# Optimization experiments

Measured on AMD Instinct MI355X. Metric: run time of the kernel, lower is better.

The kernel has to match this reference:

```python
import jax, jax.numpy as jnp
import numpy as np

B, L, D, H = 2, 2048, 512, 8
DK = D // H
NEG = -1e18


def setup_inputs() -> dict:
    key = jax.random.key(0)
    ks = jax.random.split(key, 8)
    q = jax.random.normal(ks[0], (B, L, D), dtype=jnp.float32)
    k = jax.random.normal(ks[1], (B, L, D), dtype=jnp.float32)
    v = jax.random.normal(ks[2], (B, L, D), dtype=jnp.float32)
    mask = jax.random.bernoulli(ks[3], 0.1, (B, L, L))  # True = masked
    # qkv_combined: Linear(D, 3D); proj: Linear(D, D). Stored as (in, out).
    W_qkv = jax.random.normal(ks[4], (D, 3 * D), dtype=jnp.float32) / np.sqrt(D)
    b_qkv = jax.random.normal(ks[5], (3 * D,), dtype=jnp.float32) * 0.02
    W_proj = jax.random.normal(ks[6], (D, D), dtype=jnp.float32) / np.sqrt(D)
    b_proj = jax.random.normal(ks[7], (D,), dtype=jnp.float32) * 0.02
    return {"q": q, "k": k, "v": v, "mask": mask,
            "W_qkv": W_qkv, "b_qkv": b_qkv, "W_proj": W_proj, "b_proj": b_proj}


def reference(q, k, v, mask, W_qkv, b_qkv, W_proj, b_proj):
    # NOTE: original module ignores k, v args; Q/K/V all come from q.
    temper = jnp.sqrt(jnp.float32(D))  # sqrt(model_dim), NOT sqrt(d_k)
    qkv = q @ W_qkv + b_qkv                      # [B, L, 3D]
    qq, kk, vv = jnp.split(qkv, 3, axis=-1)      # each [B, L, D]
    # chunk along last dim into H heads then stack at dim 0 -> [H, B, L, DK]
    def split_heads(x):
        return jnp.transpose(x.reshape(B, L, H, DK), (2, 0, 1, 3))
    qh, kh, vh = split_heads(qq), split_heads(kk), split_heads(vv)
    attn = jnp.einsum('hbqd,hbkd->hbqk', qh, kh) / temper  # [H, B, L, L]
    attn = jnp.where(mask[None], NEG, attn)
    attn = jax.nn.softmax(attn, axis=-1)
    out = jnp.einsum('hbqk,hbkd->hbqd', attn, vh)          # [H, B, L, DK]
    # cat heads along last dim -> [B, L, D]
    out = jnp.transpose(out, (1, 2, 0, 3)).reshape(B, L, D)
    out = out @ W_proj + b_proj
    attns = attn.reshape(H * B, L, L)
    return out, attns
```

## Files before the change

kernel.cpp:

```cpp
#include <hip/hip_runtime.h>
#include <hip/hip_bf16.h>
#include <cstdint>
#include <cstddef>

typedef __bf16 bf16_t;
typedef __attribute__((ext_vector_type(4))) __bf16 bf16x4;
typedef __attribute__((ext_vector_type(8))) __bf16 bf16x8;
typedef __attribute__((ext_vector_type(4))) float f32x4;

#define MFMA16(a, b, c) __builtin_amdgcn_mfma_f32_16x16x32_bf16(a, b, c, 0, 0, 0)

constexpr int LSEQ = 2048;
constexpr int DMODEL = 512;
constexpr int NHEAD = 8;
constexpr int DKH = 64;
constexpr float INV_TEMPER = 0.04419417382415922f;

__global__ __launch_bounds__(256) void k_transpose_cast(const float* __restrict__ in,
                                                        bf16_t* __restrict__ out,
                                                        int K, int N) {
    __shared__ float tile[32][33];
    int n0 = blockIdx.x * 32, k0 = blockIdx.y * 32;
    int tx = threadIdx.x, ty = threadIdx.y;
#pragma unroll
    for (int i = 0; i < 4; i++)
        tile[ty + i * 8][tx] = in[(size_t)(k0 + ty + i * 8) * N + n0 + tx];
    __syncthreads();
#pragma unroll
    for (int i = 0; i < 4; i++)
        out[(size_t)(n0 + ty + i * 8) * K + k0 + tx] = (bf16_t)tile[tx][ty + i * 8];
}

template <int MODE>
__global__ __launch_bounds__(256) void k_gemm_nt(const void* __restrict__ Av,
                                                 const bf16_t* __restrict__ Bt,
                                                 const float* __restrict__ bias,
                                                 bf16_t* __restrict__ outQ,
                                                 bf16_t* __restrict__ outK,
                                                 bf16_t* __restrict__ outV,
                                                 float* __restrict__ outO, int K) {
    __shared__ bf16_t As[128 * 32];
    __shared__ bf16_t Bs[128 * 32];
    int t = threadIdx.x;
    int lane = t & 63, w = t >> 6;
    int wm = w >> 1, wn = w & 1;
    int rr = lane & 15, hq = lane >> 4;
    int m0 = blockIdx.x * 128, n0 = blockIdx.y * 128;
    int srow = t >> 2, sseg = t & 3;
    const float* gaF = (const float*)Av + (size_t)(m0 + srow) * K + sseg * 8;
    const bf16_t* gaB = (const bf16_t*)Av + (size_t)(m0 + srow) * K + sseg * 8;
    const bf16_t* gb = Bt + (size_t)(n0 + srow) * K + sseg * 8;
    f32x4 acc[4][4] = {};
    for (int k0 = 0; k0 < K; k0 += 32) {
        bf16x8 a0, a1;
        if (MODE == 0) {
            float4 l0 = *reinterpret_cast<const float4*>(gaF + k0);
            float4 h0 = *reinterpret_cast<const float4*>(gaF + k0 + 4);
            float4 l1 = *reinterpret_cast<const float4*>(gaF + (size_t)64 * K + k0);
            float4 h1 = *reinterpret_cast<const float4*>(gaF + (size_t)64 * K + k0 + 4);
            a0[0] = (bf16_t)l0.x; a0[1] = (bf16_t)l0.y; a0[2] = (bf16_t)l0.z; a0[3] = (bf16_t)l0.w;
            a0[4] = (bf16_t)h0.x; a0[5] = (bf16_t)h0.y; a0[6] = (bf16_t)h0.z; a0[7] = (bf16_t)h0.w;
            a1[0] = (bf16_t)l1.x; a1[1] = (bf16_t)l1.y; a1[2] = (bf16_t)l1.z; a1[3] = (bf16_t)l1.w;
            a1[4] = (bf16_t)h1.x; a1[5] = (bf16_t)h1.y; a1[6] = (bf16_t)h1.z; a1[7] = (bf16_t)h1.w;
        } else {
            a0 = *reinterpret_cast<const bf16x8*>(gaB + k0);
            a1 = *reinterpret_cast<const bf16x8*>(gaB + (size_t)64 * K + k0);
        }
        uint4 b0 = *reinterpret_cast<const uint4*>(gb + k0);
        uint4 b1 = *reinterpret_cast<const uint4*>(gb + (size_t)64 * K + k0);
        __syncthreads();
        *reinterpret_cast<bf16x8*>(&As[srow * 32 + sseg * 8]) = a0;
        *reinterpret_cast<bf16x8*>(&As[(srow + 64) * 32 + sseg * 8]) = a1;
        *reinterpret_cast<uint4*>(&Bs[srow * 32 + sseg * 8]) = b0;
        *reinterpret_cast<uint4*>(&Bs[(srow + 64) * 32 + sseg * 8]) = b1;
        __syncthreads();
        bf16x8 af[4], bff[4];
#pragma unroll
        for (int i = 0; i < 4; i++) {
            af[i] = *reinterpret_cast<const bf16x8*>(&As[(wm * 64 + i * 16 + rr) * 32 + hq * 8]);
            bff[i] = *reinterpret_cast<const bf16x8*>(&Bs[(wn * 64 + i * 16 + rr) * 32 + hq * 8]);
        }
#pragma unroll
        for (int mi = 0; mi < 4; mi++)
#pragma unroll
            for (int ni = 0; ni < 4; ni++)
                acc[mi][ni] = MFMA16(af[mi], bff[ni], acc[mi][ni]);
    }
#pragma unroll
    for (int mi = 0; mi < 4; mi++) {
#pragma unroll
        for (int ni = 0; ni < 4; ni++) {
            int gn = n0 + wn * 64 + ni * 16 + rr;
            float bv = bias[gn];
            int gmb = m0 + wm * 64 + mi * 16 + hq * 4;
            if (MODE == 0) {
                int which = gn >> 9;
                int hn = (gn >> 6) & 7;
                int dk = gn & 63;
                if (which == 2) {
#pragma unroll
                    for (int rg = 0; rg < 4; rg++) {
                        int gm = gmb + rg;
                        int bb = gm >> 11, ll = gm & 2047;
                        outV[(((size_t)bb * NHEAD + hn) * DKH + dk) * LSEQ + ll] =
                            (bf16_t)(acc[mi][ni][rg] + bv);
                    }
                } else {
                    bf16_t* dst = which == 0 ? outQ : outK;
                    float scale = which == 0 ? INV_TEMPER : 1.0f;
#pragma unroll
                    for (int rg = 0; rg < 4; rg++) {
                        int gm = gmb + rg;
                        int bb = gm >> 11, ll = gm & 2047;
                        float v = (acc[mi][ni][rg] + bv) * scale;
                        dst[(((size_t)bb * NHEAD + hn) * LSEQ + ll) * DKH + dk] = (bf16_t)v;
                    }
                }
            } else {
#pragma unroll
                for (int rg = 0; rg < 4; rg++) {
                    int gm = gmb + rg;
                    outO[(size_t)gm * DMODEL + gn] = acc[mi][ni][rg] + bv;
                }
            }
        }
    }
}

__global__ __launch_bounds__(256) void k_attn_f(const bf16_t* __restrict__ Qh,
                                                const bf16_t* __restrict__ Kh,
                                                const bf16_t* __restrict__ Vt,
                                                const int* __restrict__ mask,
                                                float* __restrict__ attn_out,
                                                bf16_t* __restrict__ Obf) {
    extern __shared__ char sC[];
    float* sF = (float*)sC;
    float* rowpart = (float*)(sC + 65536);
    float* invLDS = (float*)(sC + 65792);
    int t = threadIdx.x;
    int lane = t & 63, w = t >> 6;
    int rr = lane & 15, hq = lane >> 4;
    int bid = blockIdx.x;
    int h = bid & 7, b = (bid >> 3) & 1, qt = bid >> 4;
    int q0 = qt * 16;
    int bh = b * NHEAD + h;
    auto swzb = [](int x) { return x ^ (((x >> 12) & 7) << 4); };

    const bf16_t* qp = Qh + ((size_t)bh * LSEQ + q0 + rr) * DKH + hq * 8;
    bf16x8 qf0 = *reinterpret_cast<const bf16x8*>(qp);
    bf16x8 qf1 = *reinterpret_cast<const bf16x8*>(qp + 32);

    const bf16_t* kb = Kh + (size_t)bh * LSEQ * DKH;
    const int* mbase = mask + ((size_t)b * LSEQ + q0) * LSEQ;
    float rs[4] = {0.f, 0.f, 0.f, 0.f};
#pragma unroll 4
    for (int nt = 0; nt < 32; nt++) {
        int cb = w * 512 + nt * 16;
        int col = cb + rr;
        int mv[4];
#pragma unroll
        for (int i = 0; i < 4; i++)
            mv[i] = mbase[(size_t)(hq * 4 + i) * LSEQ + col];
        const bf16_t* kp = kb + (size_t)col * DKH + hq * 8;
        bf16x8 kf0 = *reinterpret_cast<const bf16x8*>(kp);
        bf16x8 kf1 = *reinterpret_cast<const bf16x8*>(kp + 32);
        f32x4 acc = {0.f, 0.f, 0.f, 0.f};
        acc = MFMA16(qf0, kf0, acc);
        acc = MFMA16(qf1, kf1, acc);
#pragma unroll
        for (int i = 0; i < 4; i++) {
            float p = mv[i] ? 0.f : __expf(acc[i]);
            rs[i] += p;
            *reinterpret_cast<bf16_t*>(sC + swzb((hq * 4 + i) * 4096 + col * 2)) = (bf16_t)p;
        }
    }
#pragma unroll
    for (int i = 0; i < 4; i++) {
        rs[i] += __shfl_xor(rs[i], 8, 16);
        rs[i] += __shfl_xor(rs[i], 4, 16);
        rs[i] += __shfl_xor(rs[i], 2, 16);
        rs[i] += __shfl_xor(rs[i], 1, 16);
    }
    if (rr == 0) {
#pragma unroll
        for (int i = 0; i < 4; i++) rowpart[w * 16 + hq * 4 + i] = rs[i];
    }
    __syncthreads();
    if (t < 16)
        invLDS[t] = 1.0f / (rowpart[t] + rowpart[16 + t] + rowpart[32 + t] + rowpart[48 + t]);
    __syncthreads();

#pragma unroll 4
    for (int i = 0; i < 32; i++) {
        int e4 = (i * 256 + t) * 4;
        int rp = e4 >> 11, cp = e4 & 2047;
        bf16x4 pv = *reinterpret_cast<bf16x4*>(sC + swzb(rp * 4096 + cp * 2));
        float inv = invLDS[rp];
        float4 ov;
        ov.x = (float)pv[0] * inv; ov.y = (float)pv[1] * inv;
        ov.z = (float)pv[2] * inv; ov.w = (float)pv[3] * inv;
        *reinterpret_cast<float4*>(attn_out +
            ((size_t)(h * 2 + b) * LSEQ + q0 + rp) * LSEQ + cp) = ov;
    }

    float inv4[4];
#pragma unroll
    for (int i = 0; i < 4; i++) inv4[i] = invLDS[hq * 4 + i];
    const bf16_t* vb = Vt + (size_t)bh * DKH * LSEQ;
    f32x4 osum[4] = {};
#pragma unroll 4
    for (int ks = 0; ks < 16; ks++) {
        int kc = w * 512 + ks * 32 + hq * 8;
        bf16x8 pa = *reinterpret_cast<bf16x8*>(sC + swzb(rr * 4096 + kc * 2));
#pragma unroll
        for (int nt = 0; nt < 4; nt++) {
            const bf16_t* vp = vb + (size_t)(nt * 16 + rr) * LSEQ + kc;
            bf16x8 vf = *reinterpret_cast<const bf16x8*>(vp);
            osum[nt] = MFMA16(pa, vf, osum[nt]);
        }
    }
    __syncthreads();
#pragma unroll
    for (int nt = 0; nt < 4; nt++)
#pragma unroll
        for (int i = 0; i < 4; i++)
            sF[w * 1024 + (hq * 4 + i) * 64 + nt * 16 + rr] = osum[nt][i] * inv4[i];
    __syncthreads();
#pragma unroll
    for (int i = 0; i < 4; i++) {
        int e = i * 256 + t;
        int orow = e >> 6, oc = e & 63;
        float v = sF[orow * 64 + oc] + sF[1024 + orow * 64 + oc] +
                  sF[2048 + orow * 64 + oc] + sF[3072 + orow * 64 + oc];
        Obf[(((size_t)b * LSEQ + q0 + orow) * NHEAD + h) * DKH + oc] = (bf16_t)v;
    }
}

extern "C" void kernel_launch(void* const* d_in, const int* in_sizes, int n_in,
                              void* d_out, int out_size, void* d_ws, size_t ws_size,
                              hipStream_t stream) {
    (void)in_sizes; (void)n_in; (void)out_size; (void)ws_size;
    const float* q = (const float*)d_in[0];
    const int* mask = (const int*)d_in[3];
    const float* W_qkv = (const float*)d_in[4];
    const float* b_qkv = (const float*)d_in[5];
    const float* W_proj = (const float*)d_in[6];
    const float* b_proj = (const float*)d_in[7];
    float* out = (float*)d_out;
    float* attn_out = out + (size_t)2 * LSEQ * DMODEL;

    char* ws = (char*)d_ws;
    bf16_t* wqkv_t = (bf16_t*)(ws);
    bf16_t* wproj_t = (bf16_t*)(ws + 1572864);
    bf16_t* Qh = (bf16_t*)(ws + 2097152);
    bf16_t* Kh = (bf16_t*)(ws + 6291456);
    bf16_t* Vt = (bf16_t*)(ws + 10485760);
    bf16_t* Obf = (bf16_t*)(ws + 14680064);

    hipFuncSetAttribute((const void*)k_attn_f,
                        hipFuncAttributeMaxDynamicSharedMemorySize, 66560);

    k_transpose_cast<<<dim3(48, 16), dim3(32, 8), 0, stream>>>(W_qkv, wqkv_t, 512, 1536);
    k_transpose_cast<<<dim3(16, 16), dim3(32, 8), 0, stream>>>(W_proj, wproj_t, 512, 512);
    k_gemm_nt<0><<<dim3(32, 12), 256, 0, stream>>>(q, wqkv_t, b_qkv, Qh, Kh, Vt, nullptr, 512);
    k_attn_f<<<2048, 256, 66560, stream>>>(Qh, Kh, Vt, mask, attn_out, Obf);
    k_gemm_nt<1><<<dim3(32, 4), 256, 0, stream>>>(Obf, wproj_t, b_proj, nullptr, nullptr, nullptr, out, 512);
}
```

Baseline: 195.1 us.

## Recompute QK^T in second pass to drop the LDS probability buffer

The attention kernel no longer stages the 16x2048 bf16 probability tile in 64KB of shared memory. A first pass computes only row sums, and a second pass recomputes QK^T, normalizes, writes attn directly from registers and feeds the probabilities straight into the PV MFMA. MFMA operands are swapped so each lane owns one row with four contiguous columns, which allows vectorized int4 mask loads and float4 attn stores. V is written in a permuted column order so that layout lines up. This cuts LDS use sharply, which should allow more resident blocks, at the cost of doubling the QK^T MFMAs and the K and mask reads.

```diff
diff --git a/kernel.cpp b/kernel.cpp
--- a/kernel.cpp
+++ b/kernel.cpp
@@ -102,7 +102,8 @@
                     for (int rg = 0; rg < 4; rg++) {
                         int gm = gmb + rg;
                         int bb = gm >> 11, ll = gm & 2047;
-                        outV[(((size_t)bb * NHEAD + hn) * DKH + dk) * LSEQ + ll] =
+                        int pos = (ll & ~31) | ((ll & 0xC) << 1) | ((ll & 0x10) >> 2) | (ll & 3);
+                        outV[(((size_t)bb * NHEAD + hn) * DKH + dk) * LSEQ + pos] =
                             (bf16_t)(acc[mi][ni][rg] + bv);
                     }
                 } else {
@@ -127,16 +128,14 @@
     }
 }
 
-__global__ __launch_bounds__(256) void k_attn_f(const bf16_t* __restrict__ Qh,
-                                                const bf16_t* __restrict__ Kh,
-                                                const bf16_t* __restrict__ Vt,
-                                                const int* __restrict__ mask,
-                                                float* __restrict__ attn_out,
-                                                bf16_t* __restrict__ Obf) {
-    extern __shared__ char sC[];
-    float* sF = (float*)sC;
-    float* rowpart = (float*)(sC + 65536);
-    float* invLDS = (float*)(sC + 65792);
+__global__ __launch_bounds__(256) void k_attn4(const bf16_t* __restrict__ Qh,
+                                               const bf16_t* __restrict__ Kh,
+                                               const bf16_t* __restrict__ Vtp,
+                                               const int* __restrict__ mask,
+                                               float* __restrict__ attn_out,
+                                               bf16_t* __restrict__ Obf) {
+    __shared__ float sO[4 * 16 * 65];
+    __shared__ float rpart[16 * 17];
     int t = threadIdx.x;
     int lane = t & 63, w = t >> 6;
     int rr = lane & 15, hq = lane >> 4;
@@ -144,94 +143,87 @@
     int h = bid & 7, b = (bid >> 3) & 1, qt = bid >> 4;
     int q0 = qt * 16;
     int bh = b * NHEAD + h;
-    auto swzb = [](int x) { return x ^ (((x >> 12) & 7) << 4); };
 
     const bf16_t* qp = Qh + ((size_t)bh * LSEQ + q0 + rr) * DKH + hq * 8;
     bf16x8 qf0 = *reinterpret_cast<const bf16x8*>(qp);
     bf16x8 qf1 = *reinterpret_cast<const bf16x8*>(qp + 32);
 
     const bf16_t* kb = Kh + (size_t)bh * LSEQ * DKH;
-    const int* mbase = mask + ((size_t)b * LSEQ + q0) * LSEQ;
-    float rs[4] = {0.f, 0.f, 0.f, 0.f};
+    const int* mrow = mask + ((size_t)b * LSEQ + q0 + rr) * LSEQ;
+
+    float rs = 0.f;
 #pragma unroll 4
     for (int nt = 0; nt < 32; nt++) {
         int cb = w * 512 + nt * 16;
-        int col = cb + rr;
-        int mv[4];
-#pragma unroll
-        for (int i = 0; i < 4; i++)
-            mv[i] = mbase[(size_t)(hq * 4 + i) * LSEQ + col];
-        const bf16_t* kp = kb + (size_t)col * DKH + hq * 8;
+        const bf16_t* kp = kb + (size_t)(cb + rr) * DKH + hq * 8;
         bf16x8 kf0 = *reinterpret_cast<const bf16x8*>(kp);
         bf16x8 kf1 = *reinterpret_cast<const bf16x8*>(kp + 32);
         f32x4 acc = {0.f, 0.f, 0.f, 0.f};
-        acc = MFMA16(qf0, kf0, acc);
-        acc = MFMA16(qf1, kf1, acc);
-#pragma unroll
-        for (int i = 0; i < 4; i++) {
-            float p = mv[i] ? 0.f : __expf(acc[i]);
-            rs[i] += p;
-            *reinterpret_cast<bf16_t*>(sC + swzb((hq * 4 + i) * 4096 + col * 2)) = (bf16_t)p;
-        }
-    }
-#pragma unroll
-    for (int i = 0; i < 4; i++) {
-        rs[i] += __shfl_xor(rs[i], 8, 16);
-        rs[i] += __shfl_xor(rs[i], 4, 16);
-        rs[i] += __shfl_xor(rs[i], 2, 16);
-        rs[i] += __shfl_xor(rs[i], 1, 16);
-    }
-    if (rr == 0) {
-#pragma unroll
-        for (int i = 0; i < 4; i++) rowpart[w * 16 + hq * 4 + i] = rs[i];
-    }
+        acc = MFMA16(kf0, qf0, acc);
+        acc = MFMA16(kf1, qf1, acc);
+        int4 mv = *reinterpret_cast<const int4*>(mrow + cb + hq * 4);
+        rs += mv.x ? 0.f : __expf(acc[0]);
+        rs += mv.y ? 0.f : __expf(acc[1]);
+        rs += mv.z ? 0.f : __expf(acc[2]);
+        rs += mv.w ? 0.f : __expf(acc[3]);
+    }
+    rpart[rr * 17 + w * 4 + hq] = rs;
     __syncthreads();
-    if (t < 16)
-        invLDS[t] = 1.0f / (rowpart[t] + rowpart[16 + t] + rowpart[32 + t] + rowpart[48 + t]);
-    __syncthreads();
-
-#pragma unroll 4
-    for (int i = 0; i < 32; i++) {
-        int e4 = (i * 256 + t) * 4;
-        int rp = e4 >> 11, cp = e4 & 2047;
-        bf16x4 pv = *reinterpret_cast<bf16x4*>(sC + swzb(rp * 4096 + cp * 2));
-        float inv = invLDS[rp];
-        float4 ov;
-        ov.x = (float)pv[0] * inv; ov.y = (float)pv[1] * inv;
-        ov.z = (float)pv[2] * inv; ov.w = (float)pv[3] * inv;
-        *reinterpret_cast<float4*>(attn_out +
-            ((size_t)(h * 2 + b) * LSEQ + q0 + rp) * LSEQ + cp) = ov;
-    }
-
-    float inv4[4];
-#pragma unroll
-    for (int i = 0; i < 4; i++) inv4[i] = invLDS[hq * 4 + i];
-    const bf16_t* vb = Vt + (size_t)bh * DKH * LSEQ;
+    float sum = 0.f;
+#pragma unroll
+    for (int j = 0; j < 16; j++) sum += rpart[rr * 17 + j];
+    float invr = 1.0f / sum;
+
+    const bf16_t* vb = Vtp + (size_t)bh * DKH * LSEQ;
+    float* arow = attn_out + ((size_t)(h * 2 + b) * LSEQ + q0 + rr) * LSEQ;
     f32x4 osum[4] = {};
-#pragma unroll 4
-    for (int ks = 0; ks < 16; ks++) {
-        int kc = w * 512 + ks * 32 + hq * 8;
-        bf16x8 pa = *reinterpret_cast<bf16x8*>(sC + swzb(rr * 4096 + kc * 2));
-#pragma unroll
-        for (int nt = 0; nt < 4; nt++) {
-            const bf16_t* vp = vb + (size_t)(nt * 16 + rr) * LSEQ + kc;
-            bf16x8 vf = *reinterpret_cast<const bf16x8*>(vp);
-            osum[nt] = MFMA16(pa, vf, osum[nt]);
-        }
-    }
-    __syncthreads();
-#pragma unroll
-    for (int nt = 0; nt < 4; nt++)
+#pragma unroll 2
+    for (int nt2 = 0; nt2 < 16; nt2++) {
+        int cb0 = w * 512 + nt2 * 32;
+        const bf16_t* kp0 = kb + (size_t)(cb0 + rr) * DKH + hq * 8;
+        const bf16_t* kp1 = kb + (size_t)(cb0 + 16 + rr) * DKH + hq * 8;
+        bf16x8 kf00 = *reinterpret_cast<const bf16x8*>(kp0);
+        bf16x8 kf01 = *reinterpret_cast<const bf16x8*>(kp0 + 32);
+        bf16x8 kf10 = *reinterpret_cast<const bf16x8*>(kp1);
+        bf16x8 kf11 = *reinterpret_cast<const bf16x8*>(kp1 + 32);
+        f32x4 a0 = {0.f, 0.f, 0.f, 0.f}, a1 = {0.f, 0.f, 0.f, 0.f};
+        a0 = MFMA16(kf00, qf0, a0); a0 = MFMA16(kf01, qf1, a0);
+        a1 = MFMA16(kf10, qf0, a1); a1 = MFMA16(kf11, qf1, a1);
+        int4 m0 = *reinterpret_cast<const int4*>(mrow + cb0 + hq * 4);
+        int4 m1 = *reinterpret_cast<const int4*>(mrow + cb0 + 16 + hq * 4);
+        float p0 = m0.x ? 0.f : __expf(a0[0]) * invr;
+        float p1 = m0.y ? 0.f : __expf(a0[1]) * invr;
+        float p2 = m0.z ? 0.f : __expf(a0[2]) * invr;
+        float p3 = m0.w ? 0.f : __expf(a0[3]) * invr;
+        float p4 = m1.x ? 0.f : __expf(a1[0]) * invr;
+        float p5 = m1.y ? 0.f : __expf(a1[1]) * invr;
+        float p6 = m1.z ? 0.f : __expf(a1[2]) * invr;
+        float p7 = m1.w ? 0.f : __expf(a1[3]) * invr;
+        float4 w0 = {p0, p1, p2, p3}, w1 = {p4, p5, p6, p7};
+        *reinterpret_cast<float4*>(arow + cb0 + hq * 4) = w0;
+        *reinterpret_cast<float4*>(arow + cb0 + 16 + hq * 4) = w1;
+        bf16x8 pa;
+        pa[0] = (bf16_t)p0; pa[1] = (bf16_t)p1; pa[2] = (bf16_t)p2; pa[3] = (bf16_t)p3;
+        pa[4] = (bf16_t)p4; pa[5] = (bf16_t)p5; pa[6] = (bf16_t)p6; pa[7] = (bf16_t)p7;
+#pragma unroll
+        for (int ntile = 0; ntile < 4; ntile++) {
+            bf16x8 vf = *reinterpret_cast<const bf16x8*>(
+                vb + (size_t)(ntile * 16 + rr) * LSEQ + cb0 + hq * 8);
+            osum[ntile] = MFMA16(vf, pa, osum[ntile]);
+        }
+    }
+#pragma unroll
+    for (int ntile = 0; ntile < 4; ntile++)
 #pragma unroll
         for (int i = 0; i < 4; i++)
-            sF[w * 1024 + (hq * 4 + i) * 64 + nt * 16 + rr] = osum[nt][i] * inv4[i];
+            sO[w * 1040 + rr * 65 + ntile * 16 + hq * 4 + i] = osum[ntile][i];
     __syncthreads();
 #pragma unroll
     for (int i = 0; i < 4; i++) {
         int e = i * 256 + t;
         int orow = e >> 6, oc = e & 63;
-        float v = sF[orow * 64 + oc] + sF[1024 + orow * 64 + oc] +
-                  sF[2048 + orow * 64 + oc] + sF[3072 + orow * 64 + oc];
+        float v = sO[orow * 65 + oc] + sO[1040 + orow * 65 + oc] +
+                  sO[2080 + orow * 65 + oc] + sO[3120 + orow * 65 + oc];
         Obf[(((size_t)b * LSEQ + q0 + orow) * NHEAD + h) * DKH + oc] = (bf16_t)v;
     }
 }
@@ -254,15 +246,12 @@
     bf16_t* wproj_t = (bf16_t*)(ws + 1572864);
     bf16_t* Qh = (bf16_t*)(ws + 2097152);
     bf16_t* Kh = (bf16_t*)(ws + 6291456);
-    bf16_t* Vt = (bf16_t*)(ws + 10485760);
+    bf16_t* Vtp = (bf16_t*)(ws + 10485760);
     bf16_t* Obf = (bf16_t*)(ws + 14680064);
-
-    hipFuncSetAttribute((const void*)k_attn_f,
-                        hipFuncAttributeMaxDynamicSharedMemorySize, 66560);
 
     k_transpose_cast<<<dim3(48, 16), dim3(32, 8), 0, stream>>>(W_qkv, wqkv_t, 512, 1536);
     k_transpose_cast<<<dim3(16, 16), dim3(32, 8), 0, stream>>>(W_proj, wproj_t, 512, 512);
-    k_gemm_nt<0><<<dim3(32, 12), 256, 0, stream>>>(q, wqkv_t, b_qkv, Qh, Kh, Vt, nullptr, 512);
-    k_attn_f<<<2048, 256, 66560, stream>>>(Qh, Kh, Vt, mask, attn_out, Obf);
+    k_gemm_nt<0><<<dim3(32, 12), 256, 0, stream>>>(q, wqkv_t, b_qkv, Qh, Kh, Vtp, nullptr, 512);
+    k_attn4<<<2048, 256, 0, stream>>>(Qh, Kh, Vtp, mask, attn_out, Obf);
     k_gemm_nt<1><<<dim3(32, 4), 256, 0, stream>>>(Obf, wproj_t, b_proj, nullptr, nullptr, nullptr, out, 512);
 }
```

New measurement: 291.8 us. 49.6% more time.
